# Kernel tuning notes

Hardware: AMD Instinct MI355X
Metric: run time of the kernel (lower is better)

The kernel has to match this reference:

```python
import jax, jax.numpy as jnp
import numpy as np

N = 400_000            # nodes
E = 8_000_000          # edges (avg degree 20)
USER, TOPIC, CAT, GROUP = 200_000, 50_000, 2_000, 30_000
UD, TD, CD, GD = 8, 8, 2, 8   # embedding dims
C = 8                  # input_channels
H = 16                 # hidden layer width
OUT = 1


def setup_inputs() -> dict:
    key = jax.random.key(0)
    ks = jax.random.split(key, 24)

    # node types in {0:user, 1:topic, 2:category, 4:group}
    t = jnp.take(jnp.array([0, 1, 2, 4], dtype=jnp.int32),
                 jax.random.randint(ks[0], (N,), 0, 4))
    # per-type vocab sizes (index 3 is an unused dummy)
    vocab = jnp.array([USER, TOPIC, CAT, 1, GROUP], dtype=jnp.int32)[t]
    i0 = jax.random.randint(ks[1], (N,), 0, 1 << 30) % vocab
    i1 = jax.random.randint(ks[2], (N,), 0, 2)  # known-user flag
    features = jnp.stack([i0, i1, t], axis=1)            # [N, 3] int32
    edges = jax.random.randint(ks[3], (2, E), 0, N)      # [2, E]

    g = lambda k, shape: 0.02 * jax.random.normal(k, shape, dtype=jnp.float32)
    return {
        "edges": edges,
        "features": features,
        "user_emb": g(ks[4], (USER, UD)),
        "known_emb": g(ks[5], (2, UD)),
        "Wu": g(ks[6], (UD, C)), "bu": g(ks[7], (C,)),
        "topic_emb": g(ks[8], (TOPIC, TD)),
        "Wt": g(ks[9], (TD, C)), "bt": g(ks[10], (C,)),
        "cat_emb": g(ks[11], (CAT, CD)),
        "Wc": g(ks[12], (CD, C)), "bc": g(ks[13], (C,)),
        "group_emb": g(ks[14], (GROUP, GD)),
        "Wg": g(ks[15], (GD, C)), "bg": g(ks[16], (C,)),
        "W0": g(ks[17], (C, H)), "b0": g(ks[18], (H,)),
        "W2": g(ks[19], (H, OUT)), "b2": g(ks[20], (OUT,)),
    }


def reference(edges, features, user_emb, known_emb, Wu, bu,
              topic_emb, Wt, bt, cat_emb, Wc, bc,
              group_emb, Wg, bg, W0, b0, W2, b2):
    t = features[:, -1]
    i0 = features[:, 0]
    i1 = features[:, 1]

    # type-specific embedding gather + ReLU + linear projection (safe-indexed)
    u = jax.nn.relu(user_emb[jnp.where(t == 0, i0, 0)]
                    + known_emb[jnp.where(t == 0, i1, 0)]) @ Wu + bu
    tp = jax.nn.relu(topic_emb[jnp.where(t == 1, i0, 0)]) @ Wt + bt
    c = jax.nn.relu(cat_emb[jnp.where(t == 2, i0, 0)]) @ Wc + bc
    g = jax.nn.relu(group_emb[jnp.where(t == 4, i0, 0)]) @ Wg + bg

    tc = t[:, None]
    x = (jnp.where(tc == 0, u, 0.0) + jnp.where(tc == 1, tp, 0.0)
         + jnp.where(tc == 2, c, 0.0) + jnp.where(tc == 4, g, 0.0))  # [N, C]

    n = x.shape[0]
    loops = jnp.arange(n, dtype=edges.dtype)
    row = jnp.concatenate([edges[0], loops])   # source (with self loops)
    col = jnp.concatenate([edges[1], loops])   # target
    deg = jax.ops.segment_sum(jnp.ones_like(col, dtype=x.dtype), col,
                              num_segments=n)
    dinv = jnp.where(deg > 0, jax.lax.rsqrt(deg), 0.0)
    norm = dinv[row] * dinv[col]               # [E+N]

    def gcn_conv(h, W, b):  # PyG GCNConv: D^-1/2 (A+I) D^-1/2 h W + b
        hw = h @ W
        agg = jax.ops.segment_sum(norm[:, None] * hw[row], col, num_segments=n)
        return agg + b

    # original forward applies layers[0] (+ReLU) then layers[-1];
    # the middle GCNConv is skipped and dropout never fires.
    h = jax.nn.relu(gcn_conv(x, W0, b0))
    return gcn_conv(h, W2, b2)
```

## Files before the change

### kernel.cpp

```cpp
#include <hip/hip_runtime.h>

#define SH 10
#define BN 1024
#define CAP 22016
#define TILE 4096
#define MAXB 512
#define NCH 8
#define CSH 16
#define AGG_NB 1024


__device__ __forceinline__ unsigned short f2bf(float f) {
    union { float f; unsigned u; } x; x.f = f;
    unsigned u = x.u + 0x7fffu + ((x.u >> 16) & 1u);
    return (unsigned short)(u >> 16);
}
__device__ __forceinline__ float u2f(unsigned u) {
    union { unsigned u; float f; } x; x.u = u;
    return x.f;
}


__global__ void k_binit(int* __restrict__ bcursor, int pbkt) {
    int b = blockIdx.x * blockDim.x + threadIdx.x;
    if (b < pbkt) bcursor[b] = b * CAP;
}

__global__ void __launch_bounds__(256)
k_part(const int* __restrict__ row, const int* __restrict__ col,
       int* __restrict__ bcursor, unsigned* __restrict__ ebuf, int e) {
    __shared__ int lcnt[MAXB];
    __shared__ int gbase[MAXB];
    int t = threadIdx.x;
    int base = blockIdx.x * TILE;
    for (int j = t; j < MAXB; j += 256) lcnt[j] = 0;
    __syncthreads();
    int myb[16]; int mylpos[16]; unsigned myv[16];
#pragma unroll
    for (int k = 0; k < 16; k++) {
        int i = base + k * 256 + t;
        if (i < e) {
            int r = row[i];
            int c = col[i];
            int b = c >> SH;
            myb[k] = b;
            myv[k] = ((unsigned)r << SH) | (unsigned)(c & (BN - 1));
            mylpos[k] = atomicAdd(&lcnt[b], 1);
        } else {
            myb[k] = -1;
        }
    }
    __syncthreads();
    for (int j = t; j < MAXB; j += 256)
        if (lcnt[j] > 0) gbase[j] = atomicAdd(&bcursor[j], lcnt[j]);
    __syncthreads();
#pragma unroll
    for (int k = 0; k < 16; k++) {
        if (myb[k] >= 0) {
            int idx = gbase[myb[k]] + mylpos[k];
            if (idx < (myb[k] + 1) * CAP) ebuf[idx] = myv[k];
        }
    }
}

__global__ void k_bscan(const int* __restrict__ bcursor, int* __restrict__ bbase, int bkt) {
    __shared__ int sd[256];
    int t = threadIdx.x;
    int i0 = t * 2, i1 = t * 2 + 1;
    int v0 = (i0 < bkt) ? (bcursor[i0] - i0 * CAP) : 0;
    int v1 = (i1 < bkt) ? (bcursor[i1] - i1 * CAP) : 0;
    int s = v0 + v1;
    sd[t] = s; __syncthreads();
    for (int off = 1; off < 256; off <<= 1) {
        int x = (t >= off) ? sd[t - off] : 0;
        __syncthreads();
        sd[t] += x;
        __syncthreads();
    }
    int run = sd[t] - s;
    if (i0 < bkt) bbase[i0] = run;
    if (i1 < bkt) bbase[i1] = run + v0;
}


__global__ void __launch_bounds__(512, 4)
k_scatB(const int* __restrict__ bcursor, const int* __restrict__ bbase,
        const unsigned* __restrict__ ebuf, unsigned short* __restrict__ csr16,
        int* __restrict__ start, float* __restrict__ dinv,
        uint2* __restrict__ chunkCnt, int n, int bkt) {
    __shared__ int lcnt[BN * NCH];
    __shared__ unsigned short stage[CAP];
    __shared__ int sd[512];
    int b = blockIdx.x;
    if (b >= bkt) return;
    int t = threadIdx.x;
    int ebase = b * CAP;
    int len = bcursor[b] - ebase;
    if (len > CAP) len = CAP;
    int cbase = bbase[b];

    for (int j = t; j < BN * NCH; j += 512) lcnt[j] = 0;
    __syncthreads();
    for (int i = t; i < len; i += 512) {
        unsigned vv = ebuf[ebase + i];
        int bin = (int)((vv & (BN - 1)) << 3) | (int)((vv >> SH) >> CSH);
        atomicAdd(&lcnt[bin], 1);
    }
    __syncthreads();
    int v[16]; int s = 0;
#pragma unroll
    for (int k = 0; k < 16; k++) { v[k] = lcnt[t * 16 + k]; s += v[k]; }
    sd[t] = s; __syncthreads();
    for (int off = 1; off < 512; off <<= 1) {
        int x = (t >= off) ? sd[t - off] : 0;
        __syncthreads();
        sd[t] += x;
        __syncthreads();
    }
    int run = sd[t] - s;
    int node0 = b << SH;
#pragma unroll
    for (int nn = 0; nn < 2; nn++) {
        int node = node0 + t * 2 + nn;
        int segbase = run;
        unsigned packA = 0, packB = 0;
        int tot = 0;
#pragma unroll
        for (int k2 = 0; k2 < 8; k2++) {
            int cc = v[nn * 8 + k2];
            lcnt[t * 16 + nn * 8 + k2] = run;
            run += cc; tot += cc;
            unsigned ccs = (unsigned)(cc > 255 ? 255 : cc);
            if (k2 < 4) packA |= ccs << (8 * k2);
            else        packB |= ccs << (8 * (k2 - 4));
        }
        if (node < n) {
            start[node] = cbase + segbase;
            dinv[node] = rsqrtf((float)tot + 1.0f);
            chunkCnt[node] = make_uint2(packA, packB);
        }
    }
    __syncthreads();
    for (int i = t; i < len; i += 512) {
        unsigned vv = ebuf[ebase + i];
        unsigned r = vv >> SH;
        int bin = (int)((vv & (BN - 1)) << 3) | (int)(r >> CSH);
        int p = atomicAdd(&lcnt[bin], 1);
        unsigned short off16 = (unsigned short)(r & 0xFFFFu);
        if (p < CAP) stage[p] = off16;
        else csr16[cbase + p] = off16;
    }
    __syncthreads();
    for (int j = t; j < len; j += 512)
        __builtin_nontemporal_store(stage[j], &csr16[cbase + j]);
}


__device__ __forceinline__ void matvec8(const float* e, const float* W, const float* b, float* x) {
#pragma unroll
    for (int c = 0; c < 8; c++) x[c] = b[c];
#pragma unroll
    for (int k = 0; k < 8; k++) {
        float r = fmaxf(e[k], 0.0f);
#pragma unroll
        for (int c = 0; c < 8; c++) x[c] = fmaf(r, W[k * 8 + c], x[c]);
    }
}

__global__ void __launch_bounds__(256)
k_node(const int* __restrict__ feat,
       const float* __restrict__ user_emb, const float* __restrict__ known_emb,
       const float* __restrict__ Wu, const float* __restrict__ bu,
       const float* __restrict__ topic_emb, const float* __restrict__ Wt, const float* __restrict__ bt,
       const float* __restrict__ cat_emb, const float* __restrict__ Wc, const float* __restrict__ bc,
       const float* __restrict__ group_emb, const float* __restrict__ Wg, const float* __restrict__ bg,
       const float* __restrict__ W0, const float* __restrict__ dinv,
       unsigned short* __restrict__ yb, int n) {
    __shared__ float sWu[64], sWt[64], sWc[64], sWg[64];
    __shared__ float sbu[8], sbt[8], sbc[8], sbg[8];
    __shared__ float sW0[128];
    int t = threadIdx.x;
    if (t < 64) {
        sWu[t] = Wu[t];
        sWt[t] = Wt[t];
        sWc[t] = (t < 16) ? Wc[t] : 0.0f;
        sWg[t] = Wg[t];
    } else if (t < 192) {
        sW0[t - 64] = W0[t - 64];
    } else if (t < 200) {
        int k = t - 192;
        sbu[k] = bu[k]; sbt[k] = bt[k]; sbc[k] = bc[k]; sbg[k] = bg[k];
    }
    __syncthreads();

    int i = blockIdx.x * blockDim.x + t;
    if (i >= n) return;

    int i0 = feat[3 * i + 0];
    int i1 = feat[3 * i + 1];
    int ty = feat[3 * i + 2];

    float x[8];
    float e[8];
    if (ty == 0) {
        const float4* u = (const float4*)(user_emb + (size_t)i0 * 8);
        const float4* kn = (const float4*)(known_emb + (size_t)i1 * 8);
        float4 a0 = u[0], a1 = u[1], k0 = kn[0], k1 = kn[1];
        e[0] = a0.x + k0.x; e[1] = a0.y + k0.y; e[2] = a0.z + k0.z; e[3] = a0.w + k0.w;
        e[4] = a1.x + k1.x; e[5] = a1.y + k1.y; e[6] = a1.z + k1.z; e[7] = a1.w + k1.w;
        matvec8(e, sWu, sbu, x);
    } else if (ty == 1) {
        const float4* u = (const float4*)(topic_emb + (size_t)i0 * 8);
        float4 a0 = u[0], a1 = u[1];
        e[0] = a0.x; e[1] = a0.y; e[2] = a0.z; e[3] = a0.w;
        e[4] = a1.x; e[5] = a1.y; e[6] = a1.z; e[7] = a1.w;
        matvec8(e, sWt, sbt, x);
    } else if (ty == 2) {
        const float2* u = (const float2*)(cat_emb + (size_t)i0 * 2);
        float2 a = u[0];
        e[0] = a.x; e[1] = a.y;
#pragma unroll
        for (int k = 2; k < 8; k++) e[k] = 0.0f;
        matvec8(e, sWc, sbc, x);
    } else if (ty == 4) {
        const float4* u = (const float4*)(group_emb + (size_t)i0 * 8);
        float4 a0 = u[0], a1 = u[1];
        e[0] = a0.x; e[1] = a0.y; e[2] = a0.z; e[3] = a0.w;
        e[4] = a1.x; e[5] = a1.y; e[6] = a1.z; e[7] = a1.w;
        matvec8(e, sWg, sbg, x);
    } else {
#pragma unroll
        for (int c = 0; c < 8; c++) x[c] = 0.0f;
    }

    float di = dinv[i];
    float yv[16];
#pragma unroll
    for (int h = 0; h < 16; h++) {
        float acc = 0.0f;
#pragma unroll
        for (int c = 0; c < 8; c++) acc = fmaf(x[c], sW0[c * 16 + h], acc);
        yv[h] = di * acc;
    }
    unsigned p[8];
#pragma unroll
    for (int k = 0; k < 8; k++)
        p[k] = (unsigned)f2bf(yv[2 * k]) | ((unsigned)f2bf(yv[2 * k + 1]) << 16);
    uint4* o = (uint4*)(yb + (size_t)i * 16);
    o[0] = make_uint4(p[0], p[1], p[2], p[3]);
    o[1] = make_uint4(p[4], p[5], p[6], p[7]);
}


__device__ __forceinline__ void upadd(uint4 v, float* a) {
    a[0] += u2f(v.x << 16); a[1] += u2f(v.x & 0xffff0000u);
    a[2] += u2f(v.y << 16); a[3] += u2f(v.y & 0xffff0000u);
    a[4] += u2f(v.z << 16); a[5] += u2f(v.z & 0xffff0000u);
    a[6] += u2f(v.w << 16); a[7] += u2f(v.w & 0xffff0000u);
}

__global__ void __launch_bounds__(256, 4)
k_agg1(const int* __restrict__ start, const uint2* __restrict__ chunkCnt,
       const unsigned short* __restrict__ csr16, const uint4* __restrict__ y4,
       const float* __restrict__ dinv, const float* __restrict__ b0,
       const float* __restrict__ W2, float* __restrict__ y2, int n, int nPerBlk) {
    int t = threadIdx.x;
    int j = t & 1;
    int p = t >> 1;
    int base = blockIdx.x * nPerBlk;
    int end = base + nPerBlk; if (end > n) end = n;

    float acc[4][8];
    int cur[4]; int nd[4];
    unsigned cc0[4], cc1[4];
#pragma unroll
    for (int k = 0; k < 4; k++) {
        int node = base + p + k * 128;
        nd[k] = node;
#pragma unroll
        for (int ch = 0; ch < 8; ch++) acc[k][ch] = 0.0f;
        if (node < end) {
            cur[k] = start[node];
            uint2 cc = chunkCnt[node];
            cc0[k] = cc.x; cc1[k] = cc.y;
            upadd(y4[(size_t)node * 2 + j], acc[k]);
        } else {
            cur[k] = 0; cc0[k] = 0; cc1[k] = 0;
        }
    }

    for (int c = 0; c < 7; c++) {
        int sh = (c & 3) * 8;
        size_t hi = ((size_t)c << (CSH + 1)) + j;
#pragma unroll
        for (int k = 0; k < 4; k++) {
            unsigned packed = (c < 4) ? cc0[k] : cc1[k];
            int cc = (int)((packed >> sh) & 255u);
            int s = cur[k];
            cur[k] = s + cc;
            int i = 0;
            for (; i + 2 <= cc; i += 2) {
                int o0 = csr16[s + i];
                int o1 = csr16[s + i + 1];
                uint4 v0 = y4[hi + ((size_t)o0 << 1)];
                uint4 v1 = y4[hi + ((size_t)o1 << 1)];
                upadd(v0, acc[k]); upadd(v1, acc[k]);
            }
            if (i < cc) {
                int o = csr16[s + i];
                upadd(y4[hi + ((size_t)o << 1)], acc[k]);
            }
        }
    }

    float4 bA = ((const float4*)b0)[2 * j];
    float4 bB = ((const float4*)b0)[2 * j + 1];
    float4 wA = ((const float4*)W2)[2 * j];
    float4 wB = ((const float4*)W2)[2 * j + 1];
#pragma unroll
    for (int k = 0; k < 4; k++) {
        if (nd[k] >= end) continue;
        float di = dinv[nd[k]];
        float v = 0.0f;
        v += fmaxf(fmaf(acc[k][0], di, bA.x), 0.0f) * wA.x;
        v += fmaxf(fmaf(acc[k][1], di, bA.y), 0.0f) * wA.y;
        v += fmaxf(fmaf(acc[k][2], di, bA.z), 0.0f) * wA.z;
        v += fmaxf(fmaf(acc[k][3], di, bA.w), 0.0f) * wA.w;
        v += fmaxf(fmaf(acc[k][4], di, bB.x), 0.0f) * wB.x;
        v += fmaxf(fmaf(acc[k][5], di, bB.y), 0.0f) * wB.y;
        v += fmaxf(fmaf(acc[k][6], di, bB.z), 0.0f) * wB.z;
        v += fmaxf(fmaf(acc[k][7], di, bB.w), 0.0f) * wB.w;
        v += __shfl_xor(v, 1);
        if (j == 0) y2[nd[k]] = di * v;
    }
}

__global__ void __launch_bounds__(256)
k_agg2(const int* __restrict__ start, const uint2* __restrict__ chunkCnt,
       const unsigned short* __restrict__ csr16, const float* __restrict__ y2,
       const float* __restrict__ dinv, const float* __restrict__ b2,
       float* __restrict__ out, int n) {
    int gid = blockIdx.x * blockDim.x + threadIdx.x;
    int node = gid >> 1;
    int j = gid & 1;
    if (node >= n) return;
    uint2 cc = chunkCnt[node];
    int s = start[node];
    float acc;
    int c0, c1;
    if (j == 0) {
        acc = y2[node]; c0 = 0; c1 = 4;
    } else {
        s += (int)((cc.x & 255u) + ((cc.x >> 8) & 255u) + ((cc.x >> 16) & 255u) + (cc.x >> 24));
        acc = 0.0f; c0 = 4; c1 = 7;
    }
    for (int c = c0; c < c1; c++) {
        unsigned packed = (c < 4) ? cc.x : cc.y;
        int k = (int)((packed >> ((c & 3) * 8)) & 255u);
        int base = c << CSH;
        int i = 0;
        for (; i + 2 <= k; i += 2) {
            int o0 = csr16[s + i];
            int o1 = csr16[s + i + 1];
            acc += y2[base + o0];
            acc += y2[base + o1];
        }
        if (i < k) acc += y2[base + csr16[s + i]];
        s += k;
    }
    acc += __shfl_xor(acc, 1);
    if (j == 0) out[node] = fmaf(acc, dinv[node], b2[0]);
}


static inline size_t align_up(size_t v, size_t a) { return (v + a - 1) & ~(a - 1); }

extern "C" void kernel_launch(void* const* d_in, const int* in_sizes, int n_in,
                              void* d_out, int out_size, void* d_ws, size_t ws_size,
                              hipStream_t stream) {
    const int E = in_sizes[0] / 2;
    const int N = in_sizes[1] / 3;

    const int* edges    = (const int*)d_in[0];
    const int* row      = edges;
    const int* col      = edges + E;
    const int* feat     = (const int*)d_in[1];
    const float* user_emb  = (const float*)d_in[2];
    const float* known_emb = (const float*)d_in[3];
    const float* Wu = (const float*)d_in[4];
    const float* bu = (const float*)d_in[5];
    const float* topic_emb = (const float*)d_in[6];
    const float* Wt = (const float*)d_in[7];
    const float* bt = (const float*)d_in[8];
    const float* cat_emb = (const float*)d_in[9];
    const float* Wc = (const float*)d_in[10];
    const float* bc = (const float*)d_in[11];
    const float* group_emb = (const float*)d_in[12];
    const float* Wg = (const float*)d_in[13];
    const float* bg = (const float*)d_in[14];
    const float* W0 = (const float*)d_in[15];
    const float* b0 = (const float*)d_in[16];
    const float* W2 = (const float*)d_in[17];
    const float* b2 = (const float*)d_in[18];

    float* out = (float*)d_out;

    const int BKT  = (N + BN - 1) >> SH;
    const int PBKT = (BKT + 7) & ~7;

    char* w = (char*)d_ws;
    size_t off = 0;
    int* start    = (int*)(w + off); off = align_up(off + (size_t)N * 4, 256);
    float* dinv   = (float*)(w + off); off = align_up(off + (size_t)N * 4, 256);
    float* y2     = (float*)(w + off); off = align_up(off + (size_t)N * 4, 256);
    uint2* chunkCnt = (uint2*)(w + off); off = align_up(off + (size_t)N * 8, 256);
    int* bcursor  = (int*)(w + off); off = align_up(off + MAXB * 4, 256);
    int* bbase    = (int*)(w + off); off = align_up(off + MAXB * 4, 256);
    size_t bigsz = (size_t)BKT * CAP * 4;
    if ((size_t)N * 32 > bigsz) bigsz = (size_t)N * 32;
    unsigned* ebuf      = (unsigned*)(w + off);
    unsigned short* yb  = (unsigned short*)(w + off); off = align_up(off + bigsz, 256);
    unsigned short* csr16 = (unsigned short*)(w + off); off = align_up(off + (size_t)E * 2, 256);
    (void)ws_size;

    int tb = 256;
    int gbN = (N + tb - 1) / tb;
    int ntile = (E + TILE - 1) / TILE;

    k_binit<<<(PBKT + 255) / 256, 256, 0, stream>>>(bcursor, PBKT);
    k_part<<<ntile, tb, 0, stream>>>(row, col, bcursor, ebuf, E);
    k_bscan<<<1, 256, 0, stream>>>(bcursor, bbase, BKT);
    k_scatB<<<BKT, 512, 0, stream>>>(bcursor, bbase, ebuf, csr16, start, dinv,
                                     chunkCnt, N, BKT);
    k_node<<<gbN, tb, 0, stream>>>(feat, user_emb, known_emb, Wu, bu,
                                   topic_emb, Wt, bt, cat_emb, Wc, bc,
                                   group_emb, Wg, bg, W0, dinv, yb, N);
    int nPerBlk = (N + AGG_NB - 1) / AGG_NB;
    k_agg1<<<AGG_NB, tb, 0, stream>>>(start, chunkCnt, csr16, (const uint4*)yb,
                                      dinv, b0, W2, y2, N, nPerBlk);
    int gbA22 = ((N * 2) + tb - 1) / tb;
    k_agg2<<<gbA22, tb, 0, stream>>>(start, chunkCnt, csr16, y2, dinv, b2, out, N);
}
```

Measured before the change: 269.2 us.

## Locally sort edge tile by bucket in LDS before scattering to global buffer

The partition kernel now builds a per-tile bucket histogram, prefix-scans it, and places each edge into LDS ordered by bucket. It then writes the tile to the global bucket buffer in that order, so consecutive threads write contiguous runs within each bucket. The goal is more coalesced global writes than the previous scattered per-edge stores. The cost is reading col twice, an extra scan with more barriers, and about 24KB more LDS per block, which may lower occupancy.

```diff
diff --git a/kernel.cpp b/kernel.cpp
--- a/kernel.cpp
+++ b/kernel.cpp
@@ -29,37 +29,52 @@
 __global__ void __launch_bounds__(256)
 k_part(const int* __restrict__ row, const int* __restrict__ col,
        int* __restrict__ bcursor, unsigned* __restrict__ ebuf, int e) {
-    __shared__ int lcnt[MAXB];
+    __shared__ int hcnt[MAXB];
+    __shared__ int lstart[MAXB];
     __shared__ int gbase[MAXB];
+    __shared__ int sd[256];
+    __shared__ unsigned sval[TILE];
+    __shared__ unsigned short sbkt[TILE];
     int t = threadIdx.x;
     int base = blockIdx.x * TILE;
-    for (int j = t; j < MAXB; j += 256) lcnt[j] = 0;
-    __syncthreads();
-    int myb[16]; int mylpos[16]; unsigned myv[16];
-#pragma unroll
-    for (int k = 0; k < 16; k++) {
-        int i = base + k * 256 + t;
-        if (i < e) {
-            int r = row[i];
-            int c = col[i];
-            int b = c >> SH;
-            myb[k] = b;
-            myv[k] = ((unsigned)r << SH) | (unsigned)(c & (BN - 1));
-            mylpos[k] = atomicAdd(&lcnt[b], 1);
-        } else {
-            myb[k] = -1;
-        }
-    }
-    __syncthreads();
-    for (int j = t; j < MAXB; j += 256)
-        if (lcnt[j] > 0) gbase[j] = atomicAdd(&bcursor[j], lcnt[j]);
-    __syncthreads();
-#pragma unroll
-    for (int k = 0; k < 16; k++) {
-        if (myb[k] >= 0) {
-            int idx = gbase[myb[k]] + mylpos[k];
-            if (idx < (myb[k] + 1) * CAP) ebuf[idx] = myv[k];
-        }
+    int lim = e - base; if (lim > TILE) lim = TILE;
+
+    for (int j = t; j < MAXB; j += 256) hcnt[j] = 0;
+    __syncthreads();
+    for (int i = t; i < lim; i += 256)
+        atomicAdd(&hcnt[col[base + i] >> SH], 1);
+    __syncthreads();
+    int v0 = hcnt[2 * t], v1 = hcnt[2 * t + 1];
+    int s = v0 + v1;
+    sd[t] = s; __syncthreads();
+    for (int off = 1; off < 256; off <<= 1) {
+        int x = (t >= off) ? sd[t - off] : 0;
+        __syncthreads();
+        sd[t] += x;
+        __syncthreads();
+    }
+    int run = sd[t] - s;
+    lstart[2 * t] = run;
+    lstart[2 * t + 1] = run + v0;
+    if (v0 > 0) gbase[2 * t] = atomicAdd(&bcursor[2 * t], v0);
+    if (v1 > 0) gbase[2 * t + 1] = atomicAdd(&bcursor[2 * t + 1], v1);
+    __syncthreads();
+    hcnt[2 * t] = lstart[2 * t];
+    hcnt[2 * t + 1] = lstart[2 * t + 1];
+    __syncthreads();
+    for (int i = t; i < lim; i += 256) {
+        int r = row[base + i];
+        int c = col[base + i];
+        int b = c >> SH;
+        int p = atomicAdd(&hcnt[b], 1);
+        sval[p] = ((unsigned)r << SH) | (unsigned)(c & (BN - 1));
+        sbkt[p] = (unsigned short)b;
+    }
+    __syncthreads();
+    for (int j = t; j < lim; j += 256) {
+        int b = sbkt[j];
+        int idx = gbase[b] + (j - lstart[b]);
+        if (idx < (b + 1) * CAP) ebuf[idx] = sval[j];
     }
 }
 
@@ -406,7 +421,6 @@
     float* out = (float*)d_out;
 
     const int BKT  = (N + BN - 1) >> SH;
-    const int PBKT = (BKT + 7) & ~7;
 
     char* w = (char*)d_ws;
     size_t off = 0;
@@ -427,7 +441,7 @@
     int gbN = (N + tb - 1) / tb;
     int ntile = (E + TILE - 1) / TILE;
 
-    k_binit<<<(PBKT + 255) / 256, 256, 0, stream>>>(bcursor, PBKT);
+    k_binit<<<(MAXB + 255) / 256, 256, 0, stream>>>(bcursor, MAXB);
     k_part<<<ntile, tb, 0, stream>>>(row, col, bcursor, ebuf, E);
     k_bscan<<<1, 256, 0, stream>>>(bcursor, bbase, BKT);
     k_scatB<<<BKT, 512, 0, stream>>>(bcursor, bbase, ebuf, csr16, start, dinv,
```

Measured after the change: 284.7 us. 5.8% more time.
